# Performance work log

Hardware: AMD Instinct MI355X
Metric: run time of the kernel (lower is better)

The kernel has to match this reference:

```python
import jax, jax.numpy as jnp
import numpy as np
import math

B, C, W = 4, 256, 64
GROUPS = 32
EPS = 1e-6


def setup_inputs() -> dict:
    key = jax.random.key(0)
    ks = jax.random.split(key, 6)
    xavier = math.sqrt(2.0 / (C + C))
    return {
        "x": jax.random.normal(ks[0], (B, C, W, W), dtype=jnp.float32),
        "gn_gamma": jnp.ones((C,), dtype=jnp.float32),
        "gn_beta": jnp.zeros((C,), dtype=jnp.float32),
        "wq": jax.random.normal(ks[1], (C, C), dtype=jnp.float32) * xavier,
        "bq": jnp.zeros((C,), dtype=jnp.float32),
        "wk": jax.random.normal(ks[2], (C, C), dtype=jnp.float32) * xavier,
        "bk": jnp.zeros((C,), dtype=jnp.float32),
        "wv": jax.random.normal(ks[3], (C, C), dtype=jnp.float32) * xavier,
        "bv": jnp.zeros((C,), dtype=jnp.float32),
        "wo": jax.random.normal(ks[4], (C, C), dtype=jnp.float32) * 1e-5,
        "bo": jnp.zeros((C,), dtype=jnp.float32),
    }


def _nin(w, b, t):
    # 1x1 conv via shared weights: [O,C] x [B,C,H,W] -> [B,O,H,W]
    return jnp.einsum('oc,bchw->bohw', w, t) + b[None, :, None, None]


def _group_norm(x, gamma, beta):
    b, c, h, w = x.shape
    xr = x.reshape(b, GROUPS, c // GROUPS, h, w)
    mu = xr.mean(axis=(2, 3, 4), keepdims=True)
    var = xr.var(axis=(2, 3, 4), keepdims=True)
    xn = ((xr - mu) / jnp.sqrt(var + EPS)).reshape(b, c, h, w)
    return xn * gamma[None, :, None, None] + beta[None, :, None, None]


def reference(x, gn_gamma, gn_beta, wq, bq, wk, bk, wv, bv, wo, bo):
    b, c, wdt, _ = x.shape
    n = wdt * wdt  # number of spatial tokens
    h = _group_norm(x, gn_gamma, gn_beta)
    q = _nin(wq, bq, h).reshape(b, c, n)
    k = _nin(wk, bk, h).reshape(b, c, n)
    v = _nin(wv, bv, h).reshape(b, c, n)
    scale = 1.0 / math.sqrt(c)
    scores = jnp.einsum('bcn,bcm->bnm', q, k) * scale  # [B, N, N]
    attn = jax.nn.softmax(scores, axis=-1)
    o = jnp.einsum('bnm,bcm->bcn', attn, v).reshape(b, c, wdt, wdt)
    return x + _nin(wo, bo, o)
```

## Files before the change

### kernel.cpp

```cpp
#include <hip/hip_runtime.h>
#include <math.h>

#define B_      4
#define C_      256
#define NTOK    4096
#define GROUPS_ 32
#define CPG_    8
#define EPS_    1e-6f
#define QSCALE  0.0625f
#define NSEG    4
#define KSEG    (NTOK / NSEG)
#define QB      128

typedef __attribute__((ext_vector_type(8)))  short short8v;
typedef __attribute__((ext_vector_type(4)))  float float4v;
typedef __attribute__((ext_vector_type(16))) float f32x16;
typedef __attribute__((ext_vector_type(4)))  unsigned short ushort4v;
typedef unsigned short ushort_t;

__device__ __forceinline__ ushort_t f2bf(float f) {
  union { float f; unsigned u; } v; v.f = f;
  unsigned r = (v.u + 0x7FFFu + ((v.u >> 16) & 1u)) >> 16;
  return (ushort_t)r;
}
__device__ __forceinline__ float bf2f(ushort_t u) {
  union { unsigned u; float f; } v; v.u = ((unsigned)u) << 16; return v.f;
}
__device__ __forceinline__ unsigned cvtpk(float lo, float hi) {
  unsigned r;
  asm("v_cvt_pk_bf16_f32 %0, %1, %2" : "=v"(r) : "v"(lo), "v"(hi));
  return r;
}

__device__ __forceinline__ float4v mfma16(short8v a, short8v b, float4v c) {
  return __builtin_amdgcn_mfma_f32_16x16x32_bf16(a, b, c, 0, 0, 0);
}
__device__ __forceinline__ f32x16 mfma32(short8v a, short8v b, f32x16 c) {
  return __builtin_amdgcn_mfma_f32_32x32x16_bf16(a, b, c, 0, 0, 0);
}

__device__ __forceinline__ void gld16(const ushort_t* g, ushort_t* l) {
  __builtin_amdgcn_global_load_lds(
      (const __attribute__((address_space(1))) unsigned int*)g,
      (__attribute__((address_space(3))) unsigned int*)l, 16, 0, 0);
}

__global__ __launch_bounds__(256) void gn_fused(
    const float* __restrict__ x, const float* __restrict__ gamma,
    const float* __restrict__ beta, ushort_t* __restrict__ Ht) {
  const int bg = blockIdx.x;
  const int b = bg >> 5, g = bg & 31;
  const size_t base = (size_t)bg * CPG_ * NTOK;
  const int t = threadIdx.x;

  float s = 0.f, s2 = 0.f;
  for (int i = t * 4; i < CPG_ * NTOK; i += 1024) {
    float4 v = *reinterpret_cast<const float4*>(x + base + i);
    s  += v.x + v.y + v.z + v.w;
    s2 += v.x * v.x + v.y * v.y + v.z * v.z + v.w * v.w;
  }
  #pragma unroll
  for (int m = 32; m >= 1; m >>= 1) { s += __shfl_xor(s, m); s2 += __shfl_xor(s2, m); }
  __shared__ float red[8];
  __shared__ float stats[2];
  const int wv = t >> 6;
  if ((t & 63) == 0) { red[wv] = s; red[4 + wv] = s2; }
  __syncthreads();
  if (t == 0) {
    float ts  = red[0] + red[1] + red[2] + red[3];
    float ts2 = red[4] + red[5] + red[6] + red[7];
    const float inv_n = 1.0f / (float)(CPG_ * NTOK);
    float mu  = ts * inv_n;
    float var = ts2 * inv_n - mu * mu;
    stats[0] = mu;
    stats[1] = rsqrtf(var + EPS_);
  }
  __syncthreads();
  const float mu = stats[0], rs = stats[1];

  float ga[8], be[8];
  #pragma unroll
  for (int c = 0; c < 8; ++c) {
    ga[c] = gamma[g * 8 + c] * rs;
    be[c] = beta[g * 8 + c] - mu * ga[c];
  }
  ushort_t* Hb = Ht + (size_t)b * NTOK * C_ + g * 8;
  #pragma unroll
  for (int it2 = 0; it2 < 16; ++it2) {
    const int n = t + 256 * it2;
    union { ushort_t us[8]; short8v v; } o8;
    #pragma unroll
    for (int c = 0; c < 8; ++c)
      o8.us[c] = f2bf(x[base + (size_t)c * NTOK + n] * ga[c] + be[c]);
    *reinterpret_cast<short8v*>(Hb + (size_t)n * C_) = o8.v;
  }
}

__global__ __launch_bounds__(256) void wconv(
    const float* __restrict__ wq, const float* __restrict__ wk,
    const float* __restrict__ wv, const float* __restrict__ wo,
    ushort_t* __restrict__ Wb) {
  const int m = blockIdx.y;
  const float* srcs[4] = {wq, wk, wv, wo};
  const float* s = srcs[m];
  const int i = (blockIdx.x * 256 + threadIdx.x) * 4;
  float4 v = *reinterpret_cast<const float4*>(s + i);
  ushort4v o4 = {f2bf(v.x), f2bf(v.y), f2bf(v.z), f2bf(v.w)};
  *reinterpret_cast<ushort4v*>(Wb + (size_t)m * 65536 + i) = o4;
}

__global__ __launch_bounds__(256) void nin_qkv(
    const ushort_t* __restrict__ Wb, const float* __restrict__ bq,
    const float* __restrict__ bk, const float* __restrict__ bv,
    const ushort_t* __restrict__ Hin,
    ushort_t* __restrict__ Qt, ushort_t* __restrict__ Kt,
    ushort_t* __restrict__ Vv) {
  const int b  = blockIdx.y;
  const int n0 = blockIdx.x * 32;
  const int t  = threadIdx.x;
  const int w  = t >> 6, l = t & 63;
  const int lg = l >> 4, ln = l & 15;
  __shared__ __align__(16) ushort_t Hs[32][264];
  const ushort_t* Hb = Hin + (size_t)b * NTOK * C_;
  #pragma unroll
  for (int it = 0; it < 4; ++it) {
    const int idx = t + 256 * it;
    const int row = idx >> 5;
    const int ch  = (idx & 31) * 8;
    *reinterpret_cast<short8v*>(&Hs[row][ch]) =
        *reinterpret_cast<const short8v*>(Hb + (size_t)(n0 + row) * C_ + ch);
  }
  __syncthreads();

  auto gemm = [&](const ushort_t* W, float4v acc[4][2]) {
    #pragma unroll
    for (int mt = 0; mt < 4; ++mt)
      #pragma unroll
      for (int nt = 0; nt < 2; ++nt) acc[mt][nt] = (float4v){0.f, 0.f, 0.f, 0.f};
    const ushort_t* Wrow = W + (size_t)(64 * w + ln) * C_;
    #pragma unroll
    for (int kk = 0; kk < 8; ++kk) {
      short8v af[4], bfr[2];
      #pragma unroll
      for (int mt = 0; mt < 4; ++mt)
        af[mt] = *reinterpret_cast<const short8v*>(Wrow + mt * 16 * C_ + kk * 32 + 8 * lg);
      #pragma unroll
      for (int nt = 0; nt < 2; ++nt)
        bfr[nt] = *reinterpret_cast<const short8v*>(&Hs[nt * 16 + ln][kk * 32 + 8 * lg]);
      #pragma unroll
      for (int mt = 0; mt < 4; ++mt)
        #pragma unroll
        for (int nt = 0; nt < 2; ++nt)
          acc[mt][nt] = mfma16(af[mt], bfr[nt], acc[mt][nt]);
    }
  };

  float4v acc[4][2];
  #pragma unroll
  for (int m = 0; m < 2; ++m) {
    const float* bias = (m == 0) ? bq : bk;
    const float osc = (m == 0) ? QSCALE : 1.0f;
    ushort_t* dst = (m == 0) ? Qt : Kt;
    gemm(Wb + (size_t)m * 65536, acc);
    #pragma unroll
    for (int mt = 0; mt < 4; ++mt) {
      const int mb = 64 * w + mt * 16 + 4 * lg;
      #pragma unroll
      for (int nt = 0; nt < 2; ++nt) {
        const int n = n0 + nt * 16 + ln;
        ushort4v pk;
        #pragma unroll
        for (int r = 0; r < 4; ++r)
          pk[r] = f2bf((acc[mt][nt][r] + bias[mb + r]) * osc);
        *reinterpret_cast<ushort4v*>(dst + ((size_t)b * NTOK + n) * C_ + mb) = pk;
      }
    }
  }
  gemm(Wb + 2 * 65536, acc);
  #pragma unroll
  for (int mt = 0; mt < 4; ++mt) {
    const int mb = 64 * w + mt * 16 + 4 * lg;
    #pragma unroll
    for (int nt = 0; nt < 2; ++nt) {
      const int n = n0 + nt * 16 + ln;
      const int k  = n & 31, kb = n >> 5;
      const int e  = (k & 3) | (((k >> 3) & 1) << 2);
      const int o  = ((k >> 2) & 1) | (((k >> 4) & 1) << 1);
      #pragma unroll
      for (int r = 0; r < 4; ++r) {
        const int c = mb + r;
        const int s = o ^ ((c >> 1) & 3);
        Vv[((size_t)b * (NTOK / 32) + kb) * (C_ * 32) + (size_t)c * 32 + s * 8 + e] =
            f2bf(acc[mt][nt][r] + bv[mb + r]);
      }
    }
  }
}

__global__ __launch_bounds__(256, 2) void flash9(
    const ushort_t* __restrict__ Qt, const ushort_t* __restrict__ Kt,
    const ushort_t* __restrict__ Vg, ushort_t* __restrict__ O0,
    ushort_t* __restrict__ Orest, float2* __restrict__ ml) {
  const int id  = blockIdx.x;
  const int xcd = id & 7, sq = id >> 3;
  const int combo = xcd + 8 * (sq >> 5);
  const int b   = combo & 3;
  const int seg = combo >> 2;
  const int q0  = (sq & 31) * QB;
  const int t = threadIdx.x, w = t >> 6, l = t & 63;
  const int ln = l & 31, hi = l >> 5;

  __shared__ __align__(16) ushort_t Ks[2][32][256];
  __shared__ __align__(16) ushort_t Vs[2][8192];

  const ushort_t* Kb_ = Kt + (size_t)b * NTOK * C_;
  const ushort_t* Vb_ = Vg + (size_t)b * NTOK * C_;

  short8v qf[16];
  {
    const ushort_t* qrow = Qt + ((size_t)b * NTOK + q0 + 32 * w + ln) * C_ + 8 * hi;
    #pragma unroll
    for (int kk = 0; kk < 16; ++kk)
      qf[kk] = *reinterpret_cast<const short8v*>(qrow + 16 * kk);
  }

  f32x16 Oacc[8];
  #pragma unroll
  for (int ct = 0; ct < 8; ++ct)
    #pragma unroll
    for (int r = 0; r < 16; ++r) Oacc[ct][r] = 0.f;
  float m_run = -1e30f, l_run = 0.f;

  const int kbase = seg * KSEG;
  const int NT = KSEG / 32;

  auto STAGE_K = [&](int buf, int k0) {
    #pragma unroll
    for (int j = 0; j < 4; ++j) {
      const int i   = 4 * w + j;
      const int row = 2 * i + (l >> 5);
      const int nn  = (l & 31) ^ (row & 15);
      gld16(Kb_ + (size_t)(k0 + row) * C_ + 8 * nn, &Ks[buf][2 * i][0]);
    }
  };
  auto STAGE_V = [&](int buf, int k0) {
    const ushort_t* vt = Vb_ + (size_t)(k0 >> 5) * (C_ * 32);
    #pragma unroll
    for (int j = 0; j < 4; ++j) {
      const int i = 4 * w + j;
      gld16(vt + i * 512 + 8 * l, &Vs[buf][i * 512]);
    }
  };

  int cur = 0;
  STAGE_K(0, kbase);
  STAGE_V(0, kbase);

  for (int it = 0; it < NT; ++it) {
    asm volatile("s_waitcnt vmcnt(4)" ::: "memory");
    __builtin_amdgcn_sched_barrier(0);
    __syncthreads();
    const bool pre = (it + 1 < NT);
    if (pre) {
      const int nxt = kbase + 32 * (it + 1);
      STAGE_K(cur ^ 1, nxt);
      STAGE_V(cur ^ 1, nxt);
    }

    f32x16 sA, sB;
    #pragma unroll
    for (int r = 0; r < 16; ++r) { sA[r] = 0.f; sB[r] = 0.f; }
    const ushort_t* Kc = &Ks[cur][0][0];
    __builtin_amdgcn_s_setprio(1);
    #pragma unroll
    for (int kk = 0; kk < 16; kk += 2) {
      short8v k0f = *reinterpret_cast<const short8v*>(
          Kc + ln * 256 + 8 * ((2 * kk + hi) ^ (ln & 15)));
      short8v k1f = *reinterpret_cast<const short8v*>(
          Kc + ln * 256 + 8 * ((2 * kk + 2 + hi) ^ (ln & 15)));
      sA = mfma32(k0f, qf[kk], sA);
      sB = mfma32(k1f, qf[kk + 1], sB);
    }
    __builtin_amdgcn_s_setprio(0);
    f32x16 sacc = sA + sB;

    float mx8[8];
    #pragma unroll
    for (int j = 0; j < 8; ++j) mx8[j] = fmaxf(sacc[j], sacc[j + 8]);
    #pragma unroll
    for (int j = 0; j < 4; ++j) mx8[j] = fmaxf(mx8[j], mx8[j + 4]);
    float pmax = fmaxf(fmaxf(mx8[0], mx8[2]), fmaxf(mx8[1], mx8[3]));
    pmax = fmaxf(pmax, __shfl_xor(pmax, 32));
    if (!__all(pmax - m_run <= 8.0f)) {
      const float mnew = fmaxf(m_run, pmax);
      const float alpha = __expf(m_run - mnew);
      m_run = mnew;
      l_run *= alpha;
      float av[16];
      #pragma unroll
      for (int r = 0; r < 16; ++r)
        av[r] = __shfl(alpha, (r & 3) + 8 * (r >> 2) + 4 * hi);
      #pragma unroll
      for (int ct = 0; ct < 8; ++ct)
        #pragma unroll
        for (int r = 0; r < 16; ++r) Oacc[ct][r] *= av[r];
    }
    float sm8[8];
    #pragma unroll
    for (int r = 0; r < 16; ++r) sacc[r] = __expf(sacc[r] - m_run);
    #pragma unroll
    for (int j = 0; j < 8; ++j) sm8[j] = sacc[j] + sacc[j + 8];
    #pragma unroll
    for (int j = 0; j < 4; ++j) sm8[j] += sm8[j + 4];
    float ps = (sm8[0] + sm8[2]) + (sm8[1] + sm8[3]);
    ps += __shfl_xor(ps, 32);
    l_run += ps;

    union { unsigned u[4]; short8v v; } P0, P1;
    #pragma unroll
    for (int j = 0; j < 4; ++j) {
      P0.u[j] = cvtpk(sacc[2 * j], sacc[2 * j + 1]);
      P1.u[j] = cvtpk(sacc[8 + 2 * j], sacc[9 + 2 * j]);
    }
    const short8v pa0 = P0.v, pa1 = P1.v;

    if (pre) asm volatile("s_waitcnt vmcnt(8)" ::: "memory");
    else     asm volatile("s_waitcnt vmcnt(0)" ::: "memory");
    __builtin_amdgcn_sched_barrier(0);
    __syncthreads();

    const ushort_t* Vc = &Vs[cur][0];
    const int sx = (ln >> 1) & 3;
    __builtin_amdgcn_s_setprio(1);
    #pragma unroll
    for (int ct = 0; ct < 8; ++ct) {
      const int c = 32 * ct + ln;
      const ushort_t* vr = Vc + c * 32;
      short8v v0 = *reinterpret_cast<const short8v*>(vr + 8 * (hi ^ sx));
      short8v v1 = *reinterpret_cast<const short8v*>(vr + 8 * ((2 | hi) ^ sx));
      Oacc[ct] = mfma32(pa0, v0, Oacc[ct]);
      Oacc[ct] = mfma32(pa1, v1, Oacc[ct]);
    }
    __builtin_amdgcn_s_setprio(0);
    cur ^= 1;
  }

  ushort_t* Op = (seg == 0 ? O0 : Orest + (size_t)(seg - 1) * (size_t)B_ * NTOK * C_)
               + (size_t)b * NTOK * C_;
  #pragma unroll
  for (int ct = 0; ct < 8; ++ct)
    #pragma unroll
    for (int r = 0; r < 16; ++r) {
      const int qr = q0 + 32 * w + (r & 3) + 8 * (r >> 2) + 4 * hi;
      Op[(size_t)qr * C_ + 32 * ct + ln] = f2bf(Oacc[ct][r]);
    }
  if (hi == 0)
    ml[(seg * B_ + b) * NTOK + q0 + 32 * w + ln] = make_float2(m_run, l_run);
}

__global__ __launch_bounds__(256) void nin_final(
    const ushort_t* __restrict__ Wo, const float* __restrict__ bo,
    const ushort_t* __restrict__ O0, const ushort_t* __restrict__ Orest,
    const float2* __restrict__ ml, const float* __restrict__ xres,
    float* __restrict__ out) {
  const int b  = blockIdx.y;
  const int n0 = blockIdx.x * 32;
  const int t  = threadIdx.x;
  const int w  = t >> 6, l = t & 63;
  const int lg = l >> 4, ln = l & 15;
  __shared__ __align__(16) ushort_t Hs[32][264];
  const size_t SLOT = (size_t)B_ * NTOK * C_;
  #pragma unroll
  for (int it = 0; it < 4; ++it) {
    const int idx = t + 256 * it;
    const int row = idx >> 5;
    const int ch  = (idx & 31) * 8;
    const int n   = n0 + row;
    float m4[NSEG], l4[NSEG], M = -1e30f;
    #pragma unroll
    for (int s = 0; s < NSEG; ++s) {
      float2 v = ml[(s * B_ + b) * NTOK + n];
      m4[s] = v.x; l4[s] = v.y;
      M = fmaxf(M, v.x);
    }
    float L = 0.f, wsc[NSEG];
    #pragma unroll
    for (int s = 0; s < NSEG; ++s) { wsc[s] = __expf(m4[s] - M); L += wsc[s] * l4[s]; }
    const float inv = 1.0f / L;
    float acc8[8];
    #pragma unroll
    for (int j = 0; j < 8; ++j) acc8[j] = 0.f;
    #pragma unroll
    for (int s = 0; s < NSEG; ++s) {
      const ushort_t* op = (s == 0 ? O0 : Orest + (size_t)(s - 1) * SLOT);
      short8v v = *reinterpret_cast<const short8v*>(
          op + ((size_t)b * NTOK + n) * C_ + ch);
      #pragma unroll
      for (int j = 0; j < 8; ++j) acc8[j] += wsc[s] * bf2f((ushort_t)v[j]);
    }
    union { ushort_t us[8]; short8v v; } o8;
    #pragma unroll
    for (int j = 0; j < 8; ++j) o8.us[j] = f2bf(acc8[j] * inv);
    *reinterpret_cast<short8v*>(&Hs[row][ch]) = o8.v;
  }
  __syncthreads();

  float4v acc[4][2];
  #pragma unroll
  for (int mt = 0; mt < 4; ++mt)
    #pragma unroll
    for (int nt = 0; nt < 2; ++nt) acc[mt][nt] = (float4v){0.f, 0.f, 0.f, 0.f};
  const ushort_t* Wrow = Wo + (size_t)(64 * w + ln) * C_;
  #pragma unroll
  for (int kk = 0; kk < 8; ++kk) {
    short8v af[4], bfr[2];
    #pragma unroll
    for (int mt = 0; mt < 4; ++mt)
      af[mt] = *reinterpret_cast<const short8v*>(Wrow + mt * 16 * C_ + kk * 32 + 8 * lg);
    #pragma unroll
    for (int nt = 0; nt < 2; ++nt)
      bfr[nt] = *reinterpret_cast<const short8v*>(&Hs[nt * 16 + ln][kk * 32 + 8 * lg]);
    #pragma unroll
    for (int mt = 0; mt < 4; ++mt)
      #pragma unroll
      for (int nt = 0; nt < 2; ++nt)
        acc[mt][nt] = mfma16(af[mt], bfr[nt], acc[mt][nt]);
  }
  #pragma unroll
  for (int mt = 0; mt < 4; ++mt) {
    const int mb = 64 * w + mt * 16 + 4 * lg;
    #pragma unroll
    for (int nt = 0; nt < 2; ++nt) {
      const int n = n0 + nt * 16 + ln;
      #pragma unroll
      for (int r = 0; r < 4; ++r) {
        const size_t off = ((size_t)b * C_ + mb + r) * NTOK + n;
        out[off] = acc[mt][nt][r] + bo[mb + r] + xres[off];
      }
    }
  }
}

extern "C" void kernel_launch(void* const* d_in, const int* in_sizes, int n_in,
                              void* d_out, int out_size, void* d_ws, size_t ws_size,
                              hipStream_t stream) {
  (void)in_sizes; (void)n_in; (void)out_size; (void)ws_size;
  const float* x     = (const float*)d_in[0];
  const float* gamma = (const float*)d_in[1];
  const float* beta  = (const float*)d_in[2];
  const float* wq    = (const float*)d_in[3];
  const float* bq    = (const float*)d_in[4];
  const float* wk    = (const float*)d_in[5];
  const float* bk    = (const float*)d_in[6];
  const float* wv    = (const float*)d_in[7];
  const float* bv    = (const float*)d_in[8];
  const float* wo    = (const float*)d_in[9];
  const float* bo    = (const float*)d_in[10];
  float* out = (float*)d_out;

  ushort_t* ws16 = (ushort_t*)d_ws;
  const size_t SLOT = (size_t)B_ * NTOK * C_;

  ushort_t* Ht  = ws16;
  ushort_t* Qt  = ws16 + SLOT;
  ushort_t* Kt  = ws16 + 2 * SLOT;
  ushort_t* Vb  = ws16 + 3 * SLOT;
  ushort_t* OpR = ws16 + 4 * SLOT;
  ushort_t* Op0 = Ht;
  ushort_t* Wb  = ws16 + 7 * SLOT;
  float*  extra = (float*)(Wb + 4 * 65536);
  float2* mlp   = (float2*)(extra + 256);

  gn_fused<<<dim3(B_ * GROUPS_), 256, 0, stream>>>(x, gamma, beta, Ht);
  wconv<<<dim3(64, 4), 256, 0, stream>>>(wq, wk, wv, wo, Wb);

  dim3 gg(NTOK / 32, B_);
  nin_qkv<<<gg, 256, 0, stream>>>(Wb, bq, bk, bv, Ht, Qt, Kt, Vb);

  flash9<<<dim3(NSEG * B_ * (NTOK / QB)), 256, 0, stream>>>(Qt, Kt, Vb, Op0, OpR, mlp);

  nin_final<<<gg, 256, 0, stream>>>(Wb + 3 * 65536, bo, Op0, OpR, mlp, x, out);
}
```

Baseline: 165.2 us.

## Use exp2 softmax with folded log2e and collapse to one barrier per tile

Folds log2(e) into the Q scale so the softmax can use exp2f instead of __expf, and raises the lazy rescale threshold to match the base-2 domain. It also replaces the split K/V waits and two __syncthreads per iteration with a single full vmcnt(0) wait plus s_barrier at the top of each tile. Buffer indices now come from the iteration parity. Fewer barriers and cheaper exponentials are the aim, but waiting on all loads up front gives up the partial overlap where the V tile could still be arriving during QK^T.

After: 180.3 us. 9.1% more time.

```diff
diff --git a/kernel.cpp b/kernel.cpp
--- a/kernel.cpp
+++ b/kernel.cpp
@@ -7,7 +7,7 @@
 #define GROUPS_ 32
 #define CPG_    8
 #define EPS_    1e-6f
-#define QSCALE  0.0625f
+#define QSCALE  (0.0625f * 1.4426950408889634f)
 #define NSEG    4
 #define KSEG    (NTOK / NSEG)
 #define QB      128
@@ -197,7 +197,7 @@
   }
 }
 
-__global__ __launch_bounds__(256, 2) void flash9(
+__global__ __launch_bounds__(256, 2) void flash11(
     const ushort_t* __restrict__ Qt, const ushort_t* __restrict__ Kt,
     const ushort_t* __restrict__ Vg, ushort_t* __restrict__ O0,
     ushort_t* __restrict__ Orest, float2* __restrict__ ml) {
@@ -252,25 +252,23 @@
     }
   };
 
-  int cur = 0;
   STAGE_K(0, kbase);
   STAGE_V(0, kbase);
 
   for (int it = 0; it < NT; ++it) {
-    asm volatile("s_waitcnt vmcnt(4)" ::: "memory");
+    asm volatile("s_waitcnt vmcnt(0)" ::: "memory");
     __builtin_amdgcn_sched_barrier(0);
-    __syncthreads();
-    const bool pre = (it + 1 < NT);
-    if (pre) {
+    __builtin_amdgcn_s_barrier();
+    if (it + 1 < NT) {
       const int nxt = kbase + 32 * (it + 1);
-      STAGE_K(cur ^ 1, nxt);
-      STAGE_V(cur ^ 1, nxt);
+      STAGE_K((it + 1) & 1, nxt);
+      STAGE_V((it + 1) & 1, nxt);
     }
 
     f32x16 sA, sB;
     #pragma unroll
     for (int r = 0; r < 16; ++r) { sA[r] = 0.f; sB[r] = 0.f; }
-    const ushort_t* Kc = &Ks[cur][0][0];
+    const ushort_t* Kc = &Ks[it & 1][0][0];
     __builtin_amdgcn_s_setprio(1);
     #pragma unroll
     for (int kk = 0; kk < 16; kk += 2) {
@@ -291,9 +289,9 @@
     for (int j = 0; j < 4; ++j) mx8[j] = fmaxf(mx8[j], mx8[j + 4]);
     float pmax = fmaxf(fmaxf(mx8[0], mx8[2]), fmaxf(mx8[1], mx8[3]));
     pmax = fmaxf(pmax, __shfl_xor(pmax, 32));
-    if (!__all(pmax - m_run <= 8.0f)) {
+    if (!__all(pmax - m_run <= 11.0f)) {
       const float mnew = fmaxf(m_run, pmax);
-      const float alpha = __expf(m_run - mnew);
+      const float alpha = exp2f(m_run - mnew);
       m_run = mnew;
       l_run *= alpha;
       float av[16];
@@ -307,7 +305,7 @@
     }
     float sm8[8];
     #pragma unroll
-    for (int r = 0; r < 16; ++r) sacc[r] = __expf(sacc[r] - m_run);
+    for (int r = 0; r < 16; ++r) sacc[r] = exp2f(sacc[r] - m_run);
     #pragma unroll
     for (int j = 0; j < 8; ++j) sm8[j] = sacc[j] + sacc[j + 8];
     #pragma unroll
@@ -324,12 +322,7 @@
     }
     const short8v pa0 = P0.v, pa1 = P1.v;
 
-    if (pre) asm volatile("s_waitcnt vmcnt(8)" ::: "memory");
-    else     asm volatile("s_waitcnt vmcnt(0)" ::: "memory");
-    __builtin_amdgcn_sched_barrier(0);
-    __syncthreads();
-
-    const ushort_t* Vc = &Vs[cur][0];
+    const ushort_t* Vc = &Vs[it & 1][0];
     const int sx = (ln >> 1) & 3;
     __builtin_amdgcn_s_setprio(1);
     #pragma unroll
@@ -342,7 +335,6 @@
       Oacc[ct] = mfma32(pa1, v1, Oacc[ct]);
     }
     __builtin_amdgcn_s_setprio(0);
-    cur ^= 1;
   }
 
   ushort_t* Op = (seg == 0 ? O0 : Orest + (size_t)(seg - 1) * (size_t)B_ * NTOK * C_)
@@ -385,7 +377,7 @@
     }
     float L = 0.f, wsc[NSEG];
     #pragma unroll
-    for (int s = 0; s < NSEG; ++s) { wsc[s] = __expf(m4[s] - M); L += wsc[s] * l4[s]; }
+    for (int s = 0; s < NSEG; ++s) { wsc[s] = exp2f(m4[s] - M); L += wsc[s] * l4[s]; }
     const float inv = 1.0f / L;
     float acc8[8];
     #pragma unroll
@@ -477,7 +469,7 @@
   dim3 gg(NTOK / 32, B_);
   nin_qkv<<<gg, 256, 0, stream>>>(Wb, bq, bk, bv, Ht, Qt, Kt, Vb);
 
-  flash9<<<dim3(NSEG * B_ * (NTOK / QB)), 256, 0, stream>>>(Qt, Kt, Vb, Op0, OpR, mlp);
+  flash11<<<dim3(NSEG * B_ * (NTOK / QB)), 256, 0, stream>>>(Qt, Kt, Vb, Op0, OpR, mlp);
 
   nin_final<<<gg, 256, 0, stream>>>(Wb + 3 * 65536, bo, Op0, OpR, mlp, x, out);
 }
```

## Fuse GroupNorm apply into QKV projection, merge prep kernels, switch softmax to exp2

Applied to the files above, without the earlier changes.

The GroupNorm kernel now only computes per-group mean and rstd, and it is merged with the weight bf16 conversion into one prep launch. The normalize-and-convert step moves into the QKV projection kernel, which reads x directly and builds the bf16 H tile in shared memory. This removes the Ht intermediate round trip and one launch. Softmax now uses exp2 with log2(e) folded into the query scale, and the rescale threshold is adjusted to match. The transposing scalar LDS writes in the projection kernel may cause bank conflicts.

Result: no change. 167.6 us (+1.4%).

```diff
diff --git a/kernel.cpp b/kernel.cpp
--- a/kernel.cpp
+++ b/kernel.cpp
@@ -7,7 +7,7 @@
 #define GROUPS_ 32
 #define CPG_    8
 #define EPS_    1e-6f
-#define QSCALE  0.0625f
+#define QSCALE  (0.0625f * 1.4426950408889634f)
 #define NSEG    4
 #define KSEG    (NTOK / NSEG)
 #define QB      128
@@ -45,74 +45,53 @@
       (__attribute__((address_space(3))) unsigned int*)l, 16, 0, 0);
 }
 
-__global__ __launch_bounds__(256) void gn_fused(
-    const float* __restrict__ x, const float* __restrict__ gamma,
-    const float* __restrict__ beta, ushort_t* __restrict__ Ht) {
-  const int bg = blockIdx.x;
-  const int b = bg >> 5, g = bg & 31;
-  const size_t base = (size_t)bg * CPG_ * NTOK;
-  const int t = threadIdx.x;
-
-  float s = 0.f, s2 = 0.f;
-  for (int i = t * 4; i < CPG_ * NTOK; i += 1024) {
-    float4 v = *reinterpret_cast<const float4*>(x + base + i);
-    s  += v.x + v.y + v.z + v.w;
-    s2 += v.x * v.x + v.y * v.y + v.z * v.z + v.w * v.w;
-  }
-  #pragma unroll
-  for (int m = 32; m >= 1; m >>= 1) { s += __shfl_xor(s, m); s2 += __shfl_xor(s2, m); }
-  __shared__ float red[8];
-  __shared__ float stats[2];
-  const int wv = t >> 6;
-  if ((t & 63) == 0) { red[wv] = s; red[4 + wv] = s2; }
-  __syncthreads();
-  if (t == 0) {
-    float ts  = red[0] + red[1] + red[2] + red[3];
-    float ts2 = red[4] + red[5] + red[6] + red[7];
-    const float inv_n = 1.0f / (float)(CPG_ * NTOK);
-    float mu  = ts * inv_n;
-    float var = ts2 * inv_n - mu * mu;
-    stats[0] = mu;
-    stats[1] = rsqrtf(var + EPS_);
-  }
-  __syncthreads();
-  const float mu = stats[0], rs = stats[1];
-
-  float ga[8], be[8];
-  #pragma unroll
-  for (int c = 0; c < 8; ++c) {
-    ga[c] = gamma[g * 8 + c] * rs;
-    be[c] = beta[g * 8 + c] - mu * ga[c];
-  }
-  ushort_t* Hb = Ht + (size_t)b * NTOK * C_ + g * 8;
-  #pragma unroll
-  for (int it2 = 0; it2 < 16; ++it2) {
-    const int n = t + 256 * it2;
-    union { ushort_t us[8]; short8v v; } o8;
-    #pragma unroll
-    for (int c = 0; c < 8; ++c)
-      o8.us[c] = f2bf(x[base + (size_t)c * NTOK + n] * ga[c] + be[c]);
-    *reinterpret_cast<short8v*>(Hb + (size_t)n * C_) = o8.v;
-  }
-}
-
-__global__ __launch_bounds__(256) void wconv(
+__global__ __launch_bounds__(256) void prep(
+    const float* __restrict__ x,
     const float* __restrict__ wq, const float* __restrict__ wk,
     const float* __restrict__ wv, const float* __restrict__ wo,
-    ushort_t* __restrict__ Wb) {
-  const int m = blockIdx.y;
-  const float* srcs[4] = {wq, wk, wv, wo};
-  const float* s = srcs[m];
-  const int i = (blockIdx.x * 256 + threadIdx.x) * 4;
-  float4 v = *reinterpret_cast<const float4*>(s + i);
-  ushort4v o4 = {f2bf(v.x), f2bf(v.y), f2bf(v.z), f2bf(v.w)};
-  *reinterpret_cast<ushort4v*>(Wb + (size_t)m * 65536 + i) = o4;
-}
-
-__global__ __launch_bounds__(256) void nin_qkv(
+    float* __restrict__ stats, ushort_t* __restrict__ Wb) {
+  const int t = threadIdx.x;
+  if (blockIdx.x < 128) {
+    const int bg = blockIdx.x;
+    const size_t base = (size_t)bg * CPG_ * NTOK;
+    float s = 0.f, s2 = 0.f;
+    for (int i = t * 4; i < CPG_ * NTOK; i += 1024) {
+      float4 v = *reinterpret_cast<const float4*>(x + base + i);
+      s  += v.x + v.y + v.z + v.w;
+      s2 += v.x * v.x + v.y * v.y + v.z * v.z + v.w * v.w;
+    }
+    #pragma unroll
+    for (int m = 32; m >= 1; m >>= 1) { s += __shfl_xor(s, m); s2 += __shfl_xor(s2, m); }
+    __shared__ float red[8];
+    const int wv_ = t >> 6;
+    if ((t & 63) == 0) { red[wv_] = s; red[4 + wv_] = s2; }
+    __syncthreads();
+    if (t == 0) {
+      float ts  = red[0] + red[1] + red[2] + red[3];
+      float ts2 = red[4] + red[5] + red[6] + red[7];
+      const float inv_n = 1.0f / (float)(CPG_ * NTOK);
+      float mu  = ts * inv_n;
+      float var = ts2 * inv_n - mu * mu;
+      stats[bg * 2]     = mu;
+      stats[bg * 2 + 1] = rsqrtf(var + EPS_);
+    }
+  } else {
+    const int id = blockIdx.x - 128;
+    const int m = id >> 6;
+    const float* srcs[4] = {wq, wk, wv, wo};
+    const float* s = srcs[m];
+    const int i = ((id & 63) * 256 + t) * 4;
+    float4 v = *reinterpret_cast<const float4*>(s + i);
+    ushort4v o4 = {f2bf(v.x), f2bf(v.y), f2bf(v.z), f2bf(v.w)};
+    *reinterpret_cast<ushort4v*>(Wb + (size_t)m * 65536 + i) = o4;
+  }
+}
+
+__global__ __launch_bounds__(256) void qkv_gn(
     const ushort_t* __restrict__ Wb, const float* __restrict__ bq,
     const float* __restrict__ bk, const float* __restrict__ bv,
-    const ushort_t* __restrict__ Hin,
+    const float* __restrict__ x, const float* __restrict__ stats,
+    const float* __restrict__ gamma, const float* __restrict__ beta,
     ushort_t* __restrict__ Qt, ushort_t* __restrict__ Kt,
     ushort_t* __restrict__ Vv) {
   const int b  = blockIdx.y;
@@ -121,14 +100,21 @@
   const int w  = t >> 6, l = t & 63;
   const int lg = l >> 4, ln = l & 15;
   __shared__ __align__(16) ushort_t Hs[32][264];
-  const ushort_t* Hb = Hin + (size_t)b * NTOK * C_;
-  #pragma unroll
-  for (int it = 0; it < 4; ++it) {
-    const int idx = t + 256 * it;
-    const int row = idx >> 5;
-    const int ch  = (idx & 31) * 8;
-    *reinterpret_cast<short8v*>(&Hs[row][ch]) =
-        *reinterpret_cast<const short8v*>(Hb + (size_t)(n0 + row) * C_ + ch);
+  const float* xb = x + (size_t)b * C_ * NTOK;
+  #pragma unroll
+  for (int j = 0; j < 8; ++j) {
+    const int f4 = t + 256 * j;
+    const int c  = f4 >> 3;
+    const int nq = (f4 & 7) * 4;
+    float4 v = *reinterpret_cast<const float4*>(xb + (size_t)c * NTOK + n0 + nq);
+    const float mu = stats[(b * GROUPS_ + (c >> 3)) * 2];
+    const float rs = stats[(b * GROUPS_ + (c >> 3)) * 2 + 1];
+    const float ga = gamma[c] * rs;
+    const float be = beta[c] - mu * ga;
+    Hs[nq + 0][c] = f2bf(v.x * ga + be);
+    Hs[nq + 1][c] = f2bf(v.y * ga + be);
+    Hs[nq + 2][c] = f2bf(v.z * ga + be);
+    Hs[nq + 3][c] = f2bf(v.w * ga + be);
   }
   __syncthreads();
 
@@ -197,7 +183,7 @@
   }
 }
 
-__global__ __launch_bounds__(256, 2) void flash9(
+__global__ __launch_bounds__(256, 2) void flash13(
     const ushort_t* __restrict__ Qt, const ushort_t* __restrict__ Kt,
     const ushort_t* __restrict__ Vg, ushort_t* __restrict__ O0,
     ushort_t* __restrict__ Orest, float2* __restrict__ ml) {
@@ -291,9 +277,9 @@
     for (int j = 0; j < 4; ++j) mx8[j] = fmaxf(mx8[j], mx8[j + 4]);
     float pmax = fmaxf(fmaxf(mx8[0], mx8[2]), fmaxf(mx8[1], mx8[3]));
     pmax = fmaxf(pmax, __shfl_xor(pmax, 32));
-    if (!__all(pmax - m_run <= 8.0f)) {
+    if (!__all(pmax - m_run <= 11.0f)) {
       const float mnew = fmaxf(m_run, pmax);
-      const float alpha = __expf(m_run - mnew);
+      const float alpha = exp2f(m_run - mnew);
       m_run = mnew;
       l_run *= alpha;
       float av[16];
@@ -307,7 +293,7 @@
     }
     float sm8[8];
     #pragma unroll
-    for (int r = 0; r < 16; ++r) sacc[r] = __expf(sacc[r] - m_run);
+    for (int r = 0; r < 16; ++r) sacc[r] = exp2f(sacc[r] - m_run);
     #pragma unroll
     for (int j = 0; j < 8; ++j) sm8[j] = sacc[j] + sacc[j + 8];
     #pragma unroll
@@ -385,7 +371,7 @@
     }
     float L = 0.f, wsc[NSEG];
     #pragma unroll
-    for (int s = 0; s < NSEG; ++s) { wsc[s] = __expf(m4[s] - M); L += wsc[s] * l4[s]; }
+    for (int s = 0; s < NSEG; ++s) { wsc[s] = exp2f(m4[s] - M); L += wsc[s] * l4[s]; }
     const float inv = 1.0f / L;
     float acc8[8];
     #pragma unroll
@@ -461,23 +447,22 @@
   ushort_t* ws16 = (ushort_t*)d_ws;
   const size_t SLOT = (size_t)B_ * NTOK * C_;
 
-  ushort_t* Ht  = ws16;
+  ushort_t* Op0 = ws16;
   ushort_t* Qt  = ws16 + SLOT;
   ushort_t* Kt  = ws16 + 2 * SLOT;
   ushort_t* Vb  = ws16 + 3 * SLOT;
   ushort_t* OpR = ws16 + 4 * SLOT;
-  ushort_t* Op0 = Ht;
   ushort_t* Wb  = ws16 + 7 * SLOT;
-  float*  extra = (float*)(Wb + 4 * 65536);
-  float2* mlp   = (float2*)(extra + 256);
-
-  gn_fused<<<dim3(B_ * GROUPS_), 256, 0, stream>>>(x, gamma, beta, Ht);
-  wconv<<<dim3(64, 4), 256, 0, stream>>>(wq, wk, wv, wo, Wb);
+  float*  stats = (float*)(Wb + 4 * 65536);
+  float2* mlp   = (float2*)(stats + 256);
+
+  prep<<<dim3(384), 256, 0, stream>>>(x, wq, wk, wv, wo, stats, Wb);
 
   dim3 gg(NTOK / 32, B_);
-  nin_qkv<<<gg, 256, 0, stream>>>(Wb, bq, bk, bv, Ht, Qt, Kt, Vb);
-
-  flash9<<<dim3(NSEG * B_ * (NTOK / QB)), 256, 0, stream>>>(Qt, Kt, Vb, Op0, OpR, mlp);
+  qkv_gn<<<gg, 256, 0, stream>>>(Wb, bq, bk, bv, x, stats, gamma, beta,
+                                 Qt, Kt, Vb);
+
+  flash13<<<dim3(NSEG * B_ * (NTOK / QB)), 256, 0, stream>>>(Qt, Kt, Vb, Op0, OpR, mlp);
 
   nin_final<<<gg, 256, 0, stream>>>(Wb + 3 * 65536, bo, Op0, OpR, mlp, x, out);
 }
```
